# Optimization experiments

Measured on AMD Instinct MI355X. Metric: run time of the kernel, lower is better.

## Reference

```python
import jax, jax.numpy as jnp
import numpy as np

G_ORDER = 4  # params['g_order']
K = 2        # kernel == stride == 2, padding 0


def _build_filters(dw):
    # dw: [C, 1, K, K]. Rotate CCW by 90*i (torch.rot90 == jnp.rot90) for i in 0..G-1,
    # stack on dim 1 -> [C, G, 1, K, K] -> [C*G, K, K]
    rot = jnp.stack([jnp.rot90(dw, k=i, axes=(-2, -1)) for i in range(G_ORDER)], axis=1)
    return rot.reshape(dw.shape[0] * G_ORDER, K, K)


def setup_inputs() -> dict:
    key = jax.random.key(0)
    k1, k2 = jax.random.split(key)
    B, C, G, H, W = 8, 256, G_ORDER, 64, 64
    x = jax.random.normal(k1, (B, C, G, H, W), dtype=jnp.float32)
    dw = jax.random.normal(k2, (C, 1, K, K), dtype=jnp.float32) * 0.5
    return {"x": x, "dw": dw}


def reference(x, dw):
    # x: [B, C, G, H, W]; dw: [C, 1, K, K]
    B, C, G, H, W = x.shape
    f = _build_filters(dw)                     # [C*G, K, K]
    xf = x.reshape(B, C * G, H, W)
    # conv_transpose2d with stride=K, padding=0, groups=C*G, kernel KxK:
    # out[b, m, K*i+di, K*j+dj] = xf[b, m, i, j] * f[m, di, dj] (non-overlapping blocks)
    out = xf[:, :, :, None, :, None] * f[None, :, None, :, None, :]  # [B, M, H, K, W, K]
    out = out.reshape(B, C * G, H * K, W * K)
    return out.reshape(B, C, G, H * K, W * K)
```

## Files before the change

kernel.cpp:

```cpp
#include <hip/hip_runtime.h>


__global__ __launch_bounds__(256) void DepthwiseRREUp_kernel(
    const float* __restrict__ x,
    const float* __restrict__ dw,
    float* __restrict__ out) {
    const int t = blockIdx.x * blockDim.x + threadIdx.x;

    const int j2   = t & 31;
    const int rest = t >> 5;
    const int i    = rest & 63;
    const int m    = rest >> 6;
    const int cg   = m & 1023;
    const int c    = cg >> 2;
    const int g    = cg & 3;

    const float2 xv = *reinterpret_cast<const float2*>(x + ((size_t)t << 1));
    const float4 w = *reinterpret_cast<const float4*>(dw + (c << 2));

    float f00, f01, f10, f11;
    switch (g) {
        case 0:  f00 = w.x; f01 = w.y; f10 = w.z; f11 = w.w; break;
        case 1:  f00 = w.y; f01 = w.w; f10 = w.x; f11 = w.z; break;
        case 2:  f00 = w.w; f01 = w.z; f10 = w.y; f11 = w.x; break;
        default: f00 = w.z; f01 = w.x; f10 = w.w; f11 = w.y; break;
    }

    const size_t obase = (size_t)m * (128 * 128) + (size_t)(2 * i) * 128 + (j2 << 2);

    const float4 o0 = make_float4(xv.x * f00, xv.x * f01, xv.y * f00, xv.y * f01);
    const float4 o1 = make_float4(xv.x * f10, xv.x * f11, xv.y * f10, xv.y * f11);

    *reinterpret_cast<float4*>(out + obase)       = o0;
    *reinterpret_cast<float4*>(out + obase + 128) = o1;
}

extern "C" void kernel_launch(void* const* d_in, const int* in_sizes, int n_in,
                              void* d_out, int out_size, void* d_ws, size_t ws_size,
                              hipStream_t stream) {
    const float* x  = (const float*)d_in[0];
    const float* dw = (const float*)d_in[1];
    float* out      = (float*)d_out;

    const int n_threads = in_sizes[0] / 2;
    const int block = 256;
    const int grid = n_threads / block;

    DepthwiseRREUp_kernel<<<grid, block, 0, stream>>>(x, dw, out);
}
```

Before: 593.4 us.

## Process one channel plane per block with batched nontemporal loads and stores

Each block now handles a whole 64x64 input plane for one (batch, channel, group) slice: every thread issues eight loads up front, then computes and writes eight 2x2 output tiles. Filter weights and rotation selection are computed once per block instead of once per pair of elements, and nontemporal load/store builtins are used to avoid polluting the cache on this streaming workload. The trade-off is fewer blocks (8192 instead of 65536) and more registers per thread, though the kernel stays bandwidth bound.

```diff
diff --git a/kernel.cpp b/kernel.cpp
--- a/kernel.cpp
+++ b/kernel.cpp
@@ -1,23 +1,23 @@
 #include <hip/hip_runtime.h>
 
+
+typedef float f32x2 __attribute__((ext_vector_type(2)));
+typedef float f32x4 __attribute__((ext_vector_type(4)));
 
 __global__ __launch_bounds__(256) void DepthwiseRREUp_kernel(
     const float* __restrict__ x,
     const float* __restrict__ dw,
     float* __restrict__ out) {
-    const int t = blockIdx.x * blockDim.x + threadIdx.x;
+    const int m  = blockIdx.x;
+    const int cg = m & 1023;
+    const int c  = cg >> 2;
+    const int g  = cg & 3;
 
-    const int j2   = t & 31;
-    const int rest = t >> 5;
-    const int i    = rest & 63;
-    const int m    = rest >> 6;
-    const int cg   = m & 1023;
-    const int c    = cg >> 2;
-    const int g    = cg & 3;
+    const int tid = threadIdx.x;
+    const int j2  = tid & 31;
+    const int i0  = tid >> 5;
 
-    const float2 xv = *reinterpret_cast<const float2*>(x + ((size_t)t << 1));
-    const float4 w = *reinterpret_cast<const float4*>(dw + (c << 2));
-
+    const f32x4 w = *reinterpret_cast<const f32x4*>(dw + (c << 2));
     float f00, f01, f10, f11;
     switch (g) {
         case 0:  f00 = w.x; f01 = w.y; f10 = w.z; f11 = w.w; break;
@@ -26,13 +26,25 @@
         default: f00 = w.z; f01 = w.x; f10 = w.w; f11 = w.y; break;
     }
 
-    const size_t obase = (size_t)m * (128 * 128) + (size_t)(2 * i) * 128 + (j2 << 2);
+    const float* xp = x + (size_t)m * 4096 + i0 * 64 + (j2 << 1);
+    float*       op = out + (size_t)m * 16384 + (i0 << 1) * 128 + (j2 << 2);
 
-    const float4 o0 = make_float4(xv.x * f00, xv.x * f01, xv.y * f00, xv.y * f01);
-    const float4 o1 = make_float4(xv.x * f10, xv.x * f11, xv.y * f10, xv.y * f11);
+    f32x2 xv[8];
+#pragma unroll
+    for (int it = 0; it < 8; ++it) {
+        xv[it] = __builtin_nontemporal_load(
+            reinterpret_cast<const f32x2*>(xp + it * 512));
+    }
 
-    *reinterpret_cast<float4*>(out + obase)       = o0;
-    *reinterpret_cast<float4*>(out + obase + 128) = o1;
+#pragma unroll
+    for (int it = 0; it < 8; ++it) {
+        const f32x2 v = xv[it];
+        const f32x4 o0 = {v.x * f00, v.x * f01, v.y * f00, v.y * f01};
+        const f32x4 o1 = {v.x * f10, v.x * f11, v.y * f10, v.y * f11};
+        float* r = op + it * 2048;
+        __builtin_nontemporal_store(o0, reinterpret_cast<f32x4*>(r));
+        __builtin_nontemporal_store(o1, reinterpret_cast<f32x4*>(r + 128));
+    }
 }
 
 extern "C" void kernel_launch(void* const* d_in, const int* in_sizes, int n_in,
@@ -42,9 +54,6 @@
     const float* dw = (const float*)d_in[1];
     float* out      = (float*)d_out;
 
-    const int n_threads = in_sizes[0] / 2;
-    const int block = 256;
-    const int grid = n_threads / block;
-
-    DepthwiseRREUp_kernel<<<grid, block, 0, stream>>>(x, dw, out);
+    const int M = in_sizes[0] / 4096;
+    DepthwiseRREUp_kernel<<<M, 256, 0, stream>>>(x, dw, out);
 }
```

New measurement: 619.5 us. 1.04x slower.
